# Performance work log

Hardware: AMD Instinct MI355X
Metric: run time of the kernel (lower is better)

## Reference

```python
import jax, jax.numpy as jnp
import numpy as np

EOS_COEF = 0.25
NEG_FILL = -1000000.0


def move_lineup(pred_legal_mat, pred_quality_vec, target_legal_mat):
    """Vectorized equivalent of the serial torch move_lineup.

    Key insight: the 'word' encoding w = i + 64*j is a bijection on (i, j), so a
    target move word matches a predicted move word iff they occupy the SAME (i, j)
    cell.  torch.nonzero enumerates in row-major order, so the target index t_idx
    is the row-major rank among target ones, and p_idx is the row-major rank among
    predicted positives at the same cell.
    """
    B, Q = pred_quality_vec.shape
    N = 64 * 64
    t = (target_legal_mat == 1).reshape(B, N)           # [B, 4096] bool
    p = (pred_legal_mat > 0).reshape(B, N)              # [B, 4096] bool
    t_rank = jnp.cumsum(t.astype(jnp.int32), axis=1) - 1  # rank among targets
    p_rank = jnp.cumsum(p.astype(jnp.int32), axis=1) - 1  # rank among preds
    # original: match only if found in preds and p_idx < Q-1 (last slot reserved)
    valid = t & p & (p_rank < Q - 1) & (t_rank < Q)
    p_safe = jnp.clip(p_rank, 0, Q - 1)
    vals = jnp.take_along_axis(pred_quality_vec, p_safe, axis=1)  # [B, N]
    t_safe = jnp.where(valid, jnp.clip(t_rank, 0, Q - 1), Q - 1)
    rows = jnp.broadcast_to(jnp.arange(B)[:, None], (B, N))
    # scatter-max: valid ranks are unique per batch; invalid entries carry -inf
    lined = jnp.full((B, Q), NEG_FILL, pred_quality_vec.dtype)
    lined = lined.at[rows, t_safe].max(jnp.where(valid, vals, -jnp.inf))
    lined = lined.at[:, -1].set(pred_quality_vec[:, -1])
    match = jnp.zeros((B, Q), jnp.float32)
    match = match.at[rows, t_safe].max(valid.astype(jnp.float32))
    match = match.at[:, -1].set(1.0)
    return lined, match


def cross_entropy_gen(inp, target):
    # faithful to the torch version: sum over BATCH dim 0, mean over class dim
    lse = jax.scipy.special.logsumexp(inp, axis=1)                      # [B]
    tn = target / (jnp.sum(target, axis=1, keepdims=True) + 1e-10)      # [B, C]
    return jnp.mean(-jnp.sum(tn * (inp - lse[:, None]), axis=0))


def criterion(pred_legal_mat, pred_quality_vec, target_legal_mat, target_quality_vec):
    # ---- label_loss: weighted BCEWithLogits over the flattened legality map ----
    x = pred_legal_mat.reshape(-1)
    tflat = target_legal_mat.reshape(-1)
    w = jnp.where(tflat == 0, EOS_COEF, 1.0)
    bce = jnp.maximum(x, 0.0) - x * tflat + jnp.log1p(jnp.exp(-jnp.abs(x)))
    loss_labels = jnp.mean(w * bce)
    # ---- mse_score_loss ----
    lined, match = move_lineup(pred_legal_mat, pred_quality_vec, target_legal_mat)
    tq = target_quality_vec * match
    loss_ce = cross_entropy_gen(lined[:, :-1], tq[:, :-1])
    loss_mse = jnp.mean((lined[:, -1] - tq[:, -1]) ** 2)
    loss_score = loss_ce * 200.0 + loss_mse
    return jnp.stack([loss_labels, loss_score])


def setup_inputs() -> dict:
    key = jax.random.key(0)
    k1, k2, k3, k4 = jax.random.split(key, 4)
    B, Q = 4096, 256
    pred_legal_mat = jax.random.normal(k1, (B, 64, 64), jnp.float32) - 2.5
    pred_quality_vec = jax.random.normal(k2, (B, Q), jnp.float32)
    # ~33 legal target moves per board (chess-like sparsity), values in {0, 1}
    target_legal_mat = (jax.random.uniform(k3, (B, 64, 64)) < 0.008).astype(jnp.float32)
    target_quality_vec = jax.random.uniform(k4, (B, Q), jnp.float32)
    return {
        "pred_legal_mat": pred_legal_mat,
        "pred_quality_vec": pred_quality_vec,
        "target_legal_mat": target_legal_mat,
        "target_quality_vec": target_quality_vec,
    }


def reference(pred_legal_mat, pred_quality_vec, target_legal_mat, target_quality_vec):
    return criterion(pred_legal_mat, pred_quality_vec, target_legal_mat, target_quality_vec)
```

## Files before the change

kernel.cpp:

```cpp
#include <hip/hip_runtime.h>
#include <cstdint>
#include <cstddef>

#define NEG_FILL -1000000.0f

__global__ __launch_bounds__(256) void criterion_rows(
    const float* __restrict__ pred_legal,
    const float* __restrict__ pred_quality,
    const float* __restrict__ target_legal,
    const float* __restrict__ target_quality,
    float* __restrict__ partials, int B) {

    __shared__ float lined[4][256];
    __shared__ float matchv[4][256];

    const int tid = threadIdx.x;
    const int lane = tid & 63;
    const int slot = tid >> 6;
    const int row_raw = blockIdx.x * 4 + slot;
    const bool active = row_raw < B;
    const int row = active ? row_raw : (B - 1);

    #pragma unroll
    for (int k = 0; k < 4; ++k) {
        lined[slot][k * 64 + lane] = NEG_FILL;
        matchv[slot][k * 64 + lane] = 0.0f;
    }

    const float* __restrict__ xrow  = pred_legal     + (size_t)row * 4096;
    const float* __restrict__ trow  = target_legal   + (size_t)row * 4096;
    const float* __restrict__ pqrow = pred_quality   + (size_t)row * 256;
    const float* __restrict__ tqrow = target_quality + (size_t)row * 256;

    float bce = 0.0f;
    int t_base = 0, p_base = 0;
    const uint64_t lm = (1ull << lane) - 1ull;

    #pragma unroll 4
    for (int seg = 0; seg < 16; ++seg) {
        const float4 x4 = *(const float4*)(xrow + seg * 256 + lane * 4);
        const float4 t4 = *(const float4*)(trow + seg * 256 + lane * 4);
        const float xs[4] = {x4.x, x4.y, x4.z, x4.w};
        const float ts[4] = {t4.x, t4.y, t4.z, t4.w};
        uint64_t bt[4], bp[4];
        #pragma unroll
        for (int e = 0; e < 4; ++e) {
            const float x = xs[e], t = ts[e];
            const float L = __logf(1.0f + __expf(-fabsf(x)));
            bce += (t == 1.0f) ? (fmaxf(-x, 0.0f) + L)
                               : 0.25f * (fmaxf(x, 0.0f) + L);
            bt[e] = __ballot(t == 1.0f);
            bp[e] = __ballot(x > 0.0f);
        }
        #pragma unroll
        for (int e = 0; e < 4; ++e) {
            if ((ts[e] == 1.0f) && (xs[e] > 0.0f)) {
                int rt = __popcll(bt[0] & lm) + __popcll(bt[1] & lm)
                       + __popcll(bt[2] & lm) + __popcll(bt[3] & lm);
                int rp = __popcll(bp[0] & lm) + __popcll(bp[1] & lm)
                       + __popcll(bp[2] & lm) + __popcll(bp[3] & lm);
                #pragma unroll
                for (int e2 = 0; e2 < 4; ++e2) {
                    if (e2 < e) {
                        rt += (int)((bt[e2] >> lane) & 1ull);
                        rp += (int)((bp[e2] >> lane) & 1ull);
                    }
                }
                const int tr = t_base + rt;
                const int pr = p_base + rp;
                if (pr < 255 && tr < 256) {
                    lined[slot][tr]  = pqrow[pr];
                    matchv[slot][tr] = 1.0f;
                }
            }
        }
        t_base += __popcll(bt[0]) + __popcll(bt[1]) + __popcll(bt[2]) + __popcll(bt[3]);
        p_base += __popcll(bp[0]) + __popcll(bp[1]) + __popcll(bp[2]) + __popcll(bp[3]);
    }

    __syncthreads();

    float m = -3.0e38f;
    float vs[4], tqs[4];
    #pragma unroll
    for (int k = 0; k < 4; ++k) {
        const int c = k * 64 + lane;
        float v  = lined[slot][c];
        float tq = tqrow[c] * matchv[slot][c];
        if (c < 255) m = fmaxf(m, v);
        else { v = 0.0f; tq = 0.0f; }
        vs[k] = v; tqs[k] = tq;
    }
    #pragma unroll
    for (int off = 32; off > 0; off >>= 1)
        m = fmaxf(m, __shfl_xor(m, off, 64));

    float se = 0.0f, tsum = 0.0f, tv = 0.0f;
    #pragma unroll
    for (int k = 0; k < 4; ++k) {
        const int c = k * 64 + lane;
        if (c < 255) {
            se   += __expf(vs[k] - m);
            tsum += tqs[k];
            tv   += tqs[k] * vs[k];
        }
    }
    float s0 = bce, s1 = se, s2 = tsum, s3 = tv;
    #pragma unroll
    for (int off = 32; off > 0; off >>= 1) {
        s0 += __shfl_xor(s0, off, 64);
        s1 += __shfl_xor(s1, off, 64);
        s2 += __shfl_xor(s2, off, 64);
        s3 += __shfl_xor(s3, off, 64);
    }

    if (active && lane == 0) {
        const float lse  = m + __logf(s1);
        const float csum = -(s3 - lse * s2) / (s2 + 1e-10f);
        const float d    = pqrow[255] - tqrow[255];
        float4 o;
        o.x = s0;
        o.y = csum;
        o.z = d * d;
        o.w = 0.0f;
        *(float4*)(partials + (size_t)row_raw * 4) = o;
    }
}

__global__ __launch_bounds__(256) void finalize_kernel(
    const float* __restrict__ partials, float* __restrict__ out, int B) {
    const int tid = threadIdx.x;
    double s0 = 0.0, s1 = 0.0, s2 = 0.0;
    for (int r = tid; r < B; r += 256) {
        const float4 p = *(const float4*)(partials + (size_t)r * 4);
        s0 += (double)p.x; s1 += (double)p.y; s2 += (double)p.z;
    }
    #pragma unroll
    for (int off = 32; off > 0; off >>= 1) {
        s0 += __shfl_xor(s0, off, 64);
        s1 += __shfl_xor(s1, off, 64);
        s2 += __shfl_xor(s2, off, 64);
    }
    __shared__ double red[3][4];
    const int lane = tid & 63, w = tid >> 6;
    if (lane == 0) { red[0][w] = s0; red[1][w] = s1; red[2][w] = s2; }
    __syncthreads();
    if (tid == 0) {
        const double b = red[0][0] + red[0][1] + red[0][2] + red[0][3];
        const double c = red[1][0] + red[1][1] + red[1][2] + red[1][3];
        const double q = red[2][0] + red[2][1] + red[2][2] + red[2][3];
        out[0] = (float)(b / ((double)B * 4096.0));
        out[1] = (float)(200.0 * (c / 255.0) + q / (double)B);
    }
}

extern "C" void kernel_launch(void* const* d_in, const int* in_sizes, int n_in,
                              void* d_out, int out_size, void* d_ws, size_t ws_size,
                              hipStream_t stream) {
    const float* pred_legal     = (const float*)d_in[0];
    const float* pred_quality   = (const float*)d_in[1];
    const float* target_legal   = (const float*)d_in[2];
    const float* target_quality = (const float*)d_in[3];

    const int B = in_sizes[0] / 4096;

    float* partials = (float*)d_ws;

    const int grid = (B + 3) / 4;
    criterion_rows<<<grid, 256, 0, stream>>>(
        pred_legal, pred_quality, target_legal, target_quality, partials, B);
    finalize_kernel<<<1, 256, 0, stream>>>(partials, (float*)d_out, B);
}
```

Baseline: 165.9 us.

## Split each row across a full block with per-wave rank offsets

Switches from one wave per row (four rows per block) to one 256-thread block per row. Each wave scans a quarter of the 4096 cells and records candidate matches with wave-local ranks in a shared list. The list is resolved after a barrier using per-wave prefix counts, and the reductions now combine partial results across waves through shared memory. This shortens the serial per-wave scan and raises memory-level parallelism, at the cost of extra barriers, shared atomics and four times as many blocks.

```diff
diff --git a/kernel.cpp b/kernel.cpp
--- a/kernel.cpp
+++ b/kernel.cpp
@@ -3,6 +3,7 @@
 #include <cstddef>
 
 #define NEG_FILL -1000000.0f
+#define MAXE 1024
 
 __global__ __launch_bounds__(256) void criterion_rows(
     const float* __restrict__ pred_legal,
@@ -11,35 +12,38 @@
     const float* __restrict__ target_quality,
     float* __restrict__ partials, int B) {
 
-    __shared__ float lined[4][256];
-    __shared__ float matchv[4][256];
-
+    const int b = blockIdx.x;
     const int tid = threadIdx.x;
     const int lane = tid & 63;
-    const int slot = tid >> 6;
-    const int row_raw = blockIdx.x * 4 + slot;
-    const bool active = row_raw < B;
-    const int row = active ? row_raw : (B - 1);
+    const int w = tid >> 6;
 
-    #pragma unroll
-    for (int k = 0; k < 4; ++k) {
-        lined[slot][k * 64 + lane] = NEG_FILL;
-        matchv[slot][k * 64 + lane] = 0.0f;
-    }
+    __shared__ float lined[256];
+    __shared__ float matchv[256];
+    __shared__ int   cnt_t[4], cnt_p[4];
+    __shared__ int   nent;
+    __shared__ int   entries[MAXE];
+    __shared__ float red4[4][4];
+    __shared__ float redm[4];
 
-    const float* __restrict__ xrow  = pred_legal     + (size_t)row * 4096;
-    const float* __restrict__ trow  = target_legal   + (size_t)row * 4096;
-    const float* __restrict__ pqrow = pred_quality   + (size_t)row * 256;
-    const float* __restrict__ tqrow = target_quality + (size_t)row * 256;
+    lined[tid]  = NEG_FILL;
+    matchv[tid] = 0.0f;
+    if (tid == 0) nent = 0;
+    __syncthreads();
+
+    const float* __restrict__ xrow  = pred_legal     + (size_t)b * 4096;
+    const float* __restrict__ trow  = target_legal   + (size_t)b * 4096;
+    const float* __restrict__ pqrow = pred_quality   + (size_t)b * 256;
+    const float* __restrict__ tqrow = target_quality + (size_t)b * 256;
+
+    const uint64_t lm = (1ull << lane) - 1ull;
 
     float bce = 0.0f;
-    int t_base = 0, p_base = 0;
-    const uint64_t lm = (1ull << lane) - 1ull;
-
-    #pragma unroll 4
-    for (int seg = 0; seg < 16; ++seg) {
-        const float4 x4 = *(const float4*)(xrow + seg * 256 + lane * 4);
-        const float4 t4 = *(const float4*)(trow + seg * 256 + lane * 4);
+    int t_run = 0, p_run = 0;
+    #pragma unroll
+    for (int seg = 0; seg < 4; ++seg) {
+        const int cbase = w * 1024 + seg * 256 + lane * 4;
+        const float4 x4 = *(const float4*)(xrow + cbase);
+        const float4 t4 = *(const float4*)(trow + cbase);
         const float xs[4] = {x4.x, x4.y, x4.z, x4.w};
         const float ts[4] = {t4.x, t4.y, t4.z, t4.w};
         uint64_t bt[4], bp[4];
@@ -55,57 +59,65 @@
         #pragma unroll
         for (int e = 0; e < 4; ++e) {
             if ((ts[e] == 1.0f) && (xs[e] > 0.0f)) {
-                int rt = __popcll(bt[0] & lm) + __popcll(bt[1] & lm)
-                       + __popcll(bt[2] & lm) + __popcll(bt[3] & lm);
-                int rp = __popcll(bp[0] & lm) + __popcll(bp[1] & lm)
-                       + __popcll(bp[2] & lm) + __popcll(bp[3] & lm);
+                int ltr = t_run + __popcll(bt[0] & lm) + __popcll(bt[1] & lm)
+                        + __popcll(bt[2] & lm) + __popcll(bt[3] & lm);
+                int lpr = p_run + __popcll(bp[0] & lm) + __popcll(bp[1] & lm)
+                        + __popcll(bp[2] & lm) + __popcll(bp[3] & lm);
                 #pragma unroll
                 for (int e2 = 0; e2 < 4; ++e2) {
                     if (e2 < e) {
-                        rt += (int)((bt[e2] >> lane) & 1ull);
-                        rp += (int)((bp[e2] >> lane) & 1ull);
+                        ltr += (int)((bt[e2] >> lane) & 1ull);
+                        lpr += (int)((bp[e2] >> lane) & 1ull);
                     }
                 }
-                const int tr = t_base + rt;
-                const int pr = p_base + rp;
-                if (pr < 255 && tr < 256) {
-                    lined[slot][tr]  = pqrow[pr];
-                    matchv[slot][tr] = 1.0f;
+                if (ltr < 256 && lpr < 255) {
+                    const int idx = atomicAdd(&nent, 1);
+                    if (idx < MAXE)
+                        entries[idx] = (w << 16) | (ltr << 8) | lpr;
                 }
             }
         }
-        t_base += __popcll(bt[0]) + __popcll(bt[1]) + __popcll(bt[2]) + __popcll(bt[3]);
-        p_base += __popcll(bp[0]) + __popcll(bp[1]) + __popcll(bp[2]) + __popcll(bp[3]);
+        t_run += (int)(__popcll(bt[0]) + __popcll(bt[1])
+                     + __popcll(bt[2]) + __popcll(bt[3]));
+        p_run += (int)(__popcll(bp[0]) + __popcll(bp[1])
+                     + __popcll(bp[2]) + __popcll(bp[3]));
     }
-
+    if (lane == 0) { cnt_t[w] = t_run; cnt_p[w] = p_run; }
     __syncthreads();
 
-    float m = -3.0e38f;
-    float vs[4], tqs[4];
-    #pragma unroll
-    for (int k = 0; k < 4; ++k) {
-        const int c = k * 64 + lane;
-        float v  = lined[slot][c];
-        float tq = tqrow[c] * matchv[slot][c];
-        if (c < 255) m = fmaxf(m, v);
-        else { v = 0.0f; tq = 0.0f; }
-        vs[k] = v; tqs[k] = tq;
+    int ne = nent; if (ne > MAXE) ne = MAXE;
+    for (int i = tid; i < ne; i += 256) {
+        const int ent = entries[i];
+        const int ew = ent >> 16, ltr = (ent >> 8) & 0xFF, lpr = ent & 0xFF;
+        int bt0 = 0, bp0 = 0;
+        #pragma unroll
+        for (int k = 0; k < 4; ++k) {
+            if (k < ew) { bt0 += cnt_t[k]; bp0 += cnt_p[k]; }
+        }
+        const int tr = bt0 + ltr, pr = bp0 + lpr;
+        if (tr < 256 && pr < 255) {
+            lined[tr]  = pqrow[pr];
+            matchv[tr] = 1.0f;
+        }
     }
+    __syncthreads();
+
+    const int c = tid;
+    const float v  = (c < 255) ? lined[c] : -3.0e38f;
+    const float tq = (c < 255) ? tqrow[c] * matchv[c] : 0.0f;
+
+    float m = v;
     #pragma unroll
     for (int off = 32; off > 0; off >>= 1)
         m = fmaxf(m, __shfl_xor(m, off, 64));
+    if (lane == 0) redm[w] = m;
+    __syncthreads();
+    m = fmaxf(fmaxf(redm[0], redm[1]), fmaxf(redm[2], redm[3]));
 
-    float se = 0.0f, tsum = 0.0f, tv = 0.0f;
-    #pragma unroll
-    for (int k = 0; k < 4; ++k) {
-        const int c = k * 64 + lane;
-        if (c < 255) {
-            se   += __expf(vs[k] - m);
-            tsum += tqs[k];
-            tv   += tqs[k] * vs[k];
-        }
-    }
-    float s0 = bce, s1 = se, s2 = tsum, s3 = tv;
+    float s0 = bce;
+    float s1 = (c < 255) ? __expf(v - m) : 0.0f;
+    float s2 = tq;
+    float s3 = (c < 255) ? tq * v : 0.0f;
     #pragma unroll
     for (int off = 32; off > 0; off >>= 1) {
         s0 += __shfl_xor(s0, off, 64);
@@ -113,17 +125,23 @@
         s2 += __shfl_xor(s2, off, 64);
         s3 += __shfl_xor(s3, off, 64);
     }
-
-    if (active && lane == 0) {
-        const float lse  = m + __logf(s1);
-        const float csum = -(s3 - lse * s2) / (s2 + 1e-10f);
+    if (lane == 0) {
+        red4[w][0] = s0; red4[w][1] = s1; red4[w][2] = s2; red4[w][3] = s3;
+    }
+    __syncthreads();
+    if (tid == 0) {
+        float S0 = 0, S1 = 0, S2 = 0, S3 = 0;
+        #pragma unroll
+        for (int k = 0; k < 4; ++k) {
+            S0 += red4[k][0]; S1 += red4[k][1];
+            S2 += red4[k][2]; S3 += red4[k][3];
+        }
+        const float lse  = m + __logf(S1);
+        const float csum = -(S3 - lse * S2) / (S2 + 1e-10f);
         const float d    = pqrow[255] - tqrow[255];
         float4 o;
-        o.x = s0;
-        o.y = csum;
-        o.z = d * d;
-        o.w = 0.0f;
-        *(float4*)(partials + (size_t)row_raw * 4) = o;
+        o.x = S0; o.y = csum; o.z = d * d; o.w = 0.0f;
+        *(float4*)(partials + (size_t)b * 4) = o;
     }
 }
 
@@ -146,11 +164,11 @@
     if (lane == 0) { red[0][w] = s0; red[1][w] = s1; red[2][w] = s2; }
     __syncthreads();
     if (tid == 0) {
-        const double b = red[0][0] + red[0][1] + red[0][2] + red[0][3];
-        const double c = red[1][0] + red[1][1] + red[1][2] + red[1][3];
-        const double q = red[2][0] + red[2][1] + red[2][2] + red[2][3];
-        out[0] = (float)(b / ((double)B * 4096.0));
-        out[1] = (float)(200.0 * (c / 255.0) + q / (double)B);
+        const double bs = red[0][0] + red[0][1] + red[0][2] + red[0][3];
+        const double cs = red[1][0] + red[1][1] + red[1][2] + red[1][3];
+        const double qs = red[2][0] + red[2][1] + red[2][2] + red[2][3];
+        out[0] = (float)(bs / ((double)B * 4096.0));
+        out[1] = (float)(200.0 * (cs / 255.0) + qs / (double)B);
     }
 }
 
@@ -166,8 +184,7 @@
 
     float* partials = (float*)d_ws;
 
-    const int grid = (B + 3) / 4;
-    criterion_rows<<<grid, 256, 0, stream>>>(
+    criterion_rows<<<B, 256, 0, stream>>>(
         pred_legal, pred_quality, target_legal, target_quality, partials, B);
     finalize_kernel<<<1, 256, 0, stream>>>(partials, (float*)d_out, B);
 }
```

New measurement: 159.8 us. 1.04x faster.

## Keep lineup in registers, prefetch segments, and use wave-uniform match loop

Applied to the files above, without the earlier changes.

Moves the per-row lined and match arrays out of shared memory into per-lane registers and drops the block barrier, so each wave exits independently. Matches are now processed with a wave-uniform loop over the set bits of the combined ballot mask, skipping segments that have none. Input loads are software-prefetched four segments ahead, and the BCE uses raw exp2 and log builtins in a branch-free form. This targets LDS traffic, barrier stalls and load latency, at the cost of more registers, which may lower occupancy.

```diff
diff --git a/kernel.cpp b/kernel.cpp
--- a/kernel.cpp
+++ b/kernel.cpp
@@ -11,101 +11,116 @@
     const float* __restrict__ target_quality,
     float* __restrict__ partials, int B) {
 
-    __shared__ float lined[4][256];
-    __shared__ float matchv[4][256];
-
-    const int tid = threadIdx.x;
+    const int tid  = threadIdx.x;
     const int lane = tid & 63;
-    const int slot = tid >> 6;
-    const int row_raw = blockIdx.x * 4 + slot;
-    const bool active = row_raw < B;
-    const int row = active ? row_raw : (B - 1);
-
-    #pragma unroll
-    for (int k = 0; k < 4; ++k) {
-        lined[slot][k * 64 + lane] = NEG_FILL;
-        matchv[slot][k * 64 + lane] = 0.0f;
-    }
+    const int w    = tid >> 6;
+    const int row  = blockIdx.x * 4 + w;
+    if (row >= B) return;
 
     const float* __restrict__ xrow  = pred_legal     + (size_t)row * 4096;
     const float* __restrict__ trow  = target_legal   + (size_t)row * 4096;
     const float* __restrict__ pqrow = pred_quality   + (size_t)row * 256;
     const float* __restrict__ tqrow = target_quality + (size_t)row * 256;
 
+    float vs[4] = {NEG_FILL, NEG_FILL, NEG_FILL, NEG_FILL};
+    float mk[4] = {0.0f, 0.0f, 0.0f, 0.0f};
+
     float bce = 0.0f;
-    int t_base = 0, p_base = 0;
-    const uint64_t lm = (1ull << lane) - 1ull;
+    int t_run = 0, p_run = 0;
 
-    #pragma unroll 4
+    float4 xb[4], tb[4];
+    #pragma unroll
+    for (int i = 0; i < 4; ++i) {
+        xb[i] = *(const float4*)(xrow + i * 256 + lane * 4);
+        tb[i] = *(const float4*)(trow + i * 256 + lane * 4);
+    }
+
+    #pragma unroll
     for (int seg = 0; seg < 16; ++seg) {
-        const float4 x4 = *(const float4*)(xrow + seg * 256 + lane * 4);
-        const float4 t4 = *(const float4*)(trow + seg * 256 + lane * 4);
+        const float4 x4 = xb[seg & 3];
+        const float4 t4 = tb[seg & 3];
+        if (seg + 4 < 16) {
+            xb[seg & 3] = *(const float4*)(xrow + (seg + 4) * 256 + lane * 4);
+            tb[seg & 3] = *(const float4*)(trow + (seg + 4) * 256 + lane * 4);
+        }
         const float xs[4] = {x4.x, x4.y, x4.z, x4.w};
         const float ts[4] = {t4.x, t4.y, t4.z, t4.w};
+
         uint64_t bt[4], bp[4];
         #pragma unroll
         for (int e = 0; e < 4; ++e) {
             const float x = xs[e], t = ts[e];
-            const float L = __logf(1.0f + __expf(-fabsf(x)));
-            bce += (t == 1.0f) ? (fmaxf(-x, 0.0f) + L)
-                               : 0.25f * (fmaxf(x, 0.0f) + L);
+            const float a  = __builtin_fabsf(x);
+            const float p2 = __builtin_amdgcn_exp2f(a * -1.44269504f);
+            const float L  = __builtin_amdgcn_logf(1.0f + p2) * 0.69314718f;
+            const float relu = fmaxf(x, 0.0f);
+            const float wgt  = 0.25f + 0.75f * t;
+            bce += wgt * (relu - x * t + L);
             bt[e] = __ballot(t == 1.0f);
             bp[e] = __ballot(x > 0.0f);
         }
-        #pragma unroll
-        for (int e = 0; e < 4; ++e) {
-            if ((ts[e] == 1.0f) && (xs[e] > 0.0f)) {
-                int rt = __popcll(bt[0] & lm) + __popcll(bt[1] & lm)
-                       + __popcll(bt[2] & lm) + __popcll(bt[3] & lm);
-                int rp = __popcll(bp[0] & lm) + __popcll(bp[1] & lm)
-                       + __popcll(bp[2] & lm) + __popcll(bp[3] & lm);
-                #pragma unroll
-                for (int e2 = 0; e2 < 4; ++e2) {
-                    if (e2 < e) {
-                        rt += (int)((bt[e2] >> lane) & 1ull);
-                        rp += (int)((bp[e2] >> lane) & 1ull);
+
+        const uint64_t bm0 = bt[0] & bp[0], bm1 = bt[1] & bp[1];
+        const uint64_t bm2 = bt[2] & bp[2], bm3 = bt[3] & bp[3];
+        if ((bm0 | bm1 | bm2 | bm3) != 0ull) {
+            const uint64_t bms[4] = {bm0, bm1, bm2, bm3};
+            #pragma unroll
+            for (int e = 0; e < 4; ++e) {
+                uint64_t m = bms[e];
+                while (m) {
+                    const int j = (int)__builtin_ctzll(m);
+                    m &= m - 1;
+                    const uint64_t below = (j == 0) ? 0ull : ((~0ull) >> (64 - j));
+                    int tr = t_run, pr = p_run;
+                    #pragma unroll
+                    for (int e2 = 0; e2 < 4; ++e2) {
+                        tr += (int)__popcll(bt[e2] & below);
+                        pr += (int)__popcll(bp[e2] & below);
+                        if (e2 < e) {
+                            tr += (int)((bt[e2] >> j) & 1ull);
+                            pr += (int)((bp[e2] >> j) & 1ull);
+                        }
                     }
-                }
-                const int tr = t_base + rt;
-                const int pr = p_base + rp;
-                if (pr < 255 && tr < 256) {
-                    lined[slot][tr]  = pqrow[pr];
-                    matchv[slot][tr] = 1.0f;
+                    if (tr < 256 && pr < 255) {
+                        const float v = pqrow[pr];
+                        const int tslot = tr >> 6, tlane = tr & 63;
+                        const bool hit = (lane == tlane);
+                        #pragma unroll
+                        for (int k = 0; k < 4; ++k) {
+                            if (k == tslot) {
+                                vs[k] = hit ? v    : vs[k];
+                                mk[k] = hit ? 1.0f : mk[k];
+                            }
+                        }
+                    }
                 }
             }
         }
-        t_base += __popcll(bt[0]) + __popcll(bt[1]) + __popcll(bt[2]) + __popcll(bt[3]);
-        p_base += __popcll(bp[0]) + __popcll(bp[1]) + __popcll(bp[2]) + __popcll(bp[3]);
+        t_run += (int)(__popcll(bt[0]) + __popcll(bt[1])
+                     + __popcll(bt[2]) + __popcll(bt[3]));
+        p_run += (int)(__popcll(bp[0]) + __popcll(bp[1])
+                     + __popcll(bp[2]) + __popcll(bp[3]));
     }
 
-    __syncthreads();
+    float tq[4];
+    #pragma unroll
+    for (int k = 0; k < 4; ++k)
+        tq[k] = tqrow[k * 64 + lane] * mk[k];
+    if (lane == 63) { vs[3] = -3.0e38f; tq[3] = 0.0f; }
 
-    float m = -3.0e38f;
-    float vs[4], tqs[4];
-    #pragma unroll
-    for (int k = 0; k < 4; ++k) {
-        const int c = k * 64 + lane;
-        float v  = lined[slot][c];
-        float tq = tqrow[c] * matchv[slot][c];
-        if (c < 255) m = fmaxf(m, v);
-        else { v = 0.0f; tq = 0.0f; }
-        vs[k] = v; tqs[k] = tq;
-    }
+    float m = fmaxf(fmaxf(vs[0], vs[1]), fmaxf(vs[2], vs[3]));
     #pragma unroll
     for (int off = 32; off > 0; off >>= 1)
         m = fmaxf(m, __shfl_xor(m, off, 64));
 
-    float se = 0.0f, tsum = 0.0f, tv = 0.0f;
+    float s1 = 0.0f, s2 = 0.0f, s3 = 0.0f;
     #pragma unroll
     for (int k = 0; k < 4; ++k) {
-        const int c = k * 64 + lane;
-        if (c < 255) {
-            se   += __expf(vs[k] - m);
-            tsum += tqs[k];
-            tv   += tqs[k] * vs[k];
-        }
+        s1 += __builtin_amdgcn_exp2f((vs[k] - m) * 1.44269504f);
+        s2 += tq[k];
+        s3 += tq[k] * vs[k];
     }
-    float s0 = bce, s1 = se, s2 = tsum, s3 = tv;
+    float s0 = bce;
     #pragma unroll
     for (int off = 32; off > 0; off >>= 1) {
         s0 += __shfl_xor(s0, off, 64);
@@ -114,16 +129,13 @@
         s3 += __shfl_xor(s3, off, 64);
     }
 
-    if (active && lane == 0) {
-        const float lse  = m + __logf(s1);
+    if (lane == 0) {
+        const float lse  = m + __builtin_amdgcn_logf(s1) * 0.69314718f;
         const float csum = -(s3 - lse * s2) / (s2 + 1e-10f);
         const float d    = pqrow[255] - tqrow[255];
         float4 o;
-        o.x = s0;
-        o.y = csum;
-        o.z = d * d;
-        o.w = 0.0f;
-        *(float4*)(partials + (size_t)row_raw * 4) = o;
+        o.x = s0; o.y = csum; o.z = d * d; o.w = 0.0f;
+        *(float4*)(partials + (size_t)row * 4) = o;
     }
 }
 
@@ -146,11 +158,11 @@
     if (lane == 0) { red[0][w] = s0; red[1][w] = s1; red[2][w] = s2; }
     __syncthreads();
     if (tid == 0) {
-        const double b = red[0][0] + red[0][1] + red[0][2] + red[0][3];
-        const double c = red[1][0] + red[1][1] + red[1][2] + red[1][3];
-        const double q = red[2][0] + red[2][1] + red[2][2] + red[2][3];
-        out[0] = (float)(b / ((double)B * 4096.0));
-        out[1] = (float)(200.0 * (c / 255.0) + q / (double)B);
+        const double bs = red[0][0] + red[0][1] + red[0][2] + red[0][3];
+        const double cs = red[1][0] + red[1][1] + red[1][2] + red[1][3];
+        const double qs = red[2][0] + red[2][1] + red[2][2] + red[2][3];
+        out[0] = (float)(bs / ((double)B * 4096.0));
+        out[1] = (float)(200.0 * (cs / 255.0) + qs / (double)B);
     }
 }
 
```

Measured after the change: 163.5 us. No clear change (-1.4%).
